# Performance work log

Measured on AMD Instinct MI355X. Metric: run time of the kernel, lower is better.

## Reference

```python
import jax, jax.numpy as jnp
import numpy as np

# DoG parameters derived from init kwargs: sigma_low=1.0, truncate=4.0
SIGMA_LOW = 1.0
SIGMA_HIGH = 1.6  # sigma_low * 1.6
KSIZE_LOW = 9     # 2*ceil(4.0*1.0)+1
KSIZE_HIGH = 15   # 2*ceil(4.0*1.6)+1


def gaussian_kernel1d(ksize: int, sigma: float) -> jnp.ndarray:
    # Matches kornia's 1D gaussian: centered, normalized to sum 1.
    t = jnp.arange(ksize, dtype=jnp.float32) - (ksize - 1) / 2.0
    g = jnp.exp(-(t * t) / (2.0 * sigma * sigma))
    return g / jnp.sum(g)


def _conv1d_along_axis(x: jnp.ndarray, g: jnp.ndarray, axis: int) -> jnp.ndarray:
    # x: (B, C, D, H, W); depthwise 1D cross-correlation along `axis` with
    # replicate ('edge') boundary handling, as in kornia filter3d(border_type='replicate').
    C = x.shape[1]
    k = g.shape[0]
    pads = [(0, 0)] * 5
    pads[axis] = (k // 2, k // 2)
    xp = jnp.pad(x, pads, mode='edge')
    kshape = [1, 1, 1]
    kshape[axis - 2] = k
    w = jnp.tile(g.reshape(1, 1, *kshape), (C, 1, 1, 1, 1))  # (C,1,kd,kh,kw)
    return jax.lax.conv_general_dilated(
        xp, w, window_strides=(1, 1, 1), padding='VALID',
        dimension_numbers=('NCDHW', 'OIDHW', 'NCDHW'),
        feature_group_count=C)


def gaussian_blur3d(x: jnp.ndarray, sigma: float, ksize: int) -> jnp.ndarray:
    # The 3D kernel is an outer product of normalized 1D gaussians, so the
    # dense 3D convolution is exactly equal to three separable 1D passes.
    g = gaussian_kernel1d(ksize, sigma)
    for ax in (2, 3, 4):
        x = _conv1d_along_axis(x, g, ax)
    return x


def setup_inputs() -> dict:
    key = jax.random.key(0)
    x = jax.random.normal(key, (2, 1, 160, 160, 160), dtype=jnp.float32)
    return {"x": x}


def reference(x) -> jnp.ndarray:
    low_pass = gaussian_blur3d(x, SIGMA_LOW, KSIZE_LOW)
    high_pass = gaussian_blur3d(x, SIGMA_HIGH, KSIZE_HIGH)
    return low_pass - high_pass
```

## Files before the change

kernel.cpp:

```cpp
#include <hip/hip_runtime.h>
#include <math.h>

#define DIMS 160
#define PLANE (DIMS*DIMS)
#define NB 2
#define RH 7
#define RL 4
#define KH 15
#define KL 9
#define TSX 16
#define TSY 32
#define NTX (DIMS/TSX)
#define NTY (DIMS/TSY)
#define CZ 16
#define NCH (DIMS/CZ)
#define NSTEPS (CZ + 2*RH)
#define YHR (TSY + 2*RH)
#define YLR (TSY + 2*RL)
#define RAWSZ 1860
#define SH 50
#define SL 42
#define NBLK (NTX*NTY*NCH*NB)

struct DoGW { float gl[KL]; float gh[KH]; };

__device__ __forceinline__ int raw_off(int r) {
  const int x = r & 15;
  return r * 40 + ((8 * ((x >> 2) & 3) + (x & 3) - 8 * (x & 3)) & 31);
}

__global__ __launch_bounds__(512, 4)
void dog_v6(const float* __restrict__ X, float* __restrict__ out, DoGW w) {
  __shared__ float sRaw[2][RAWSZ];
  __shared__ float sXh[2][TSX * SH];
  __shared__ float sXl[2][TSX * SL];

  const int bid = blockIdx.x;
  const int xt = bid % NTX;
  const int yt = (bid / NTX) % NTY;
  const int zc = (bid / (NTX * NTY)) % NCH;
  const int b  = bid / (NTX * NTY * NCH);
  const int x0 = xt * TSX, y0 = yt * TSY, z0 = zc * CZ;
  const float* Xb = X + (size_t)b * DIMS * PLANE;
  const int tid = threadIdx.x;
  const bool xfast = (x0 >= 8) && (x0 + 24 <= DIMS);

  const bool l_on = tid < YHR * 8;
  const int lrow = tid >> 3, lq = tid & 7;
  const int lyg = min(max(y0 + lrow - RH, 0), DIMS - 1);
  const int lxb = x0 - 8 + 4 * lq;
  const int lof = raw_off(lrow) + 4 * lq;

  const bool x_on = tid < YHR * 4;
  const int xr = tid >> 2, xq = tid & 3;
  const int xof = raw_off(xr) + 4 * xq;
  const bool xlow = (xr >= 3) && (xr <= 42);

  const int cy = tid >> 4, cx = tid & 15;

  auto loadP = [&](int s, float4& v) {
    if (!l_on) return;
    const int zsrc = min(max(z0 - RH + s, 0), DIMS - 1);
    const float* rowp = Xb + ((size_t)zsrc * DIMS + lyg) * DIMS;
    if (xfast) {
      v = *(const float4*)(rowp + lxb);
    } else {
      v.x = rowp[min(max(lxb + 0, 0), DIMS - 1)];
      v.y = rowp[min(max(lxb + 1, 0), DIMS - 1)];
      v.z = rowp[min(max(lxb + 2, 0), DIMS - 1)];
      v.w = rowp[min(max(lxb + 3, 0), DIMS - 1)];
    }
  };
  auto stageP = [&](const float4& v, int buf) {
    if (!l_on) return;
    float* p = &sRaw[buf][lof];
    p[0] = v.x; p[1] = v.y; p[2] = v.z; p[3] = v.w;
  };

  float accH[KH], accL[KL + 3];
  #pragma unroll
  for (int i = 0; i < KH; ++i) accH[i] = 0.f;
  #pragma unroll
  for (int i = 0; i < KL + 3; ++i) accL[i] = 0.f;

  {
    float4 v;
    loadP(0, v);
    stageP(v, 0);
  }
  __syncthreads();

  #pragma unroll 2
  for (int s = 0; s < NSTEPS; ++s) {
    const int cur = s & 1;
    float4 vnext;
    if (s + 1 < NSTEPS) loadP(s + 1, vnext);

    if (x_on) {
      const float* p = &sRaw[cur][xof];
      float v[20];
      #pragma unroll
      for (int j = 0; j < 20; ++j) v[j] = p[j];
      #pragma unroll
      for (int c = 0; c < 4; ++c) {
        float a = 0.f;
        #pragma unroll
        for (int k = 0; k < KH; ++k) a = fmaf(w.gh[k], v[c + 1 + k], a);
        sXh[cur][(4 * xq + c) * SH + xr] = a;
      }
      if (xlow) {
        #pragma unroll
        for (int c = 0; c < 4; ++c) {
          float a = 0.f;
          #pragma unroll
          for (int k = 0; k < KL; ++k) a = fmaf(w.gl[k], v[c + 4 + k], a);
          sXl[cur][(4 * xq + c) * SL + (xr - 3)] = a;
        }
      }
    }
    if (s + 1 < NSTEPS) stageP(vnext, 1 - cur);

    __syncthreads();

    float ph = 0.f, pl = 0.f;
    #pragma unroll
    for (int j = 0; j < KH; ++j) ph = fmaf(w.gh[j], sXh[cur][cx * SH + cy + j], ph);
    #pragma unroll
    for (int j = 0; j < KL; ++j) pl = fmaf(w.gl[j], sXl[cur][cx * SL + cy + j], pl);

    #pragma unroll
    for (int i = 0; i < KH; ++i) accH[i] = fmaf(w.gh[KH - 1 - i], ph, accH[i]);
    #pragma unroll
    for (int i = 3; i < KL + 3; ++i) accL[i] = fmaf(w.gl[KL + 2 - i], pl, accL[i]);

    if (s >= 2 * RH) {
      const int zo = z0 + s - 2 * RH;
      out[((size_t)(b * DIMS + zo) * DIMS + (y0 + cy)) * DIMS + (x0 + cx)] = accL[0] - accH[0];
    }
    #pragma unroll
    for (int i = 0; i < KH - 1; ++i) accH[i] = accH[i + 1];
    accH[KH - 1] = 0.f;
    #pragma unroll
    for (int i = 0; i < KL + 2; ++i) accL[i] = accL[i + 1];
    accL[KL + 2] = 0.f;
  }
}

extern "C" void kernel_launch(void* const* d_in, const int* in_sizes, int n_in,
                              void* d_out, int out_size, void* d_ws, size_t ws_size,
                              hipStream_t stream) {
  const float* X = (const float*)d_in[0];
  float* out = (float*)d_out;

  DoGW w;
  {
    double s = 0.0;
    for (int i = 0; i < KL; ++i) {
      double t = i - (KL - 1) / 2.0;
      double g = exp(-(t * t) / (2.0 * 1.0 * 1.0));
      w.gl[i] = (float)g; s += g;
    }
    for (int i = 0; i < KL; ++i) w.gl[i] = (float)((double)w.gl[i] / s);
    s = 0.0;
    for (int i = 0; i < KH; ++i) {
      double t = i - (KH - 1) / 2.0;
      double g = exp(-(t * t) / (2.0 * 1.6 * 1.6));
      w.gh[i] = (float)g; s += g;
    }
    for (int i = 0; i < KH; ++i) w.gh[i] = (float)((double)w.gh[i] / s);
  }

  dog_v6<<<NBLK, 512, 0, stream>>>(X, out, w);
}
```

Baseline: 143.0 us.

## Software-pipeline DoG stages with two-step global prefetch and skewed consume

The z-direction (and y) consume of step s-1 now runs in the same barrier interval as the x-convolution of step s. The global load for step s+2 is also issued while step s is processed, so each global read has two iterations to land. The aim is to hide global-memory latency and to fill the idle time around the per-step barrier with independent work. The cost is one more float4 held live across iterations, plus an epilogue consume after the loop, which may raise register pressure under the 512-thread launch bound.

```diff
diff --git a/kernel.cpp b/kernel.cpp
--- a/kernel.cpp
+++ b/kernel.cpp
@@ -30,7 +30,7 @@
 }
 
 __global__ __launch_bounds__(512, 4)
-void dog_v6(const float* __restrict__ X, float* __restrict__ out, DoGW w) {
+void dog_v7(const float* __restrict__ X, float* __restrict__ out, DoGW w) {
   __shared__ float sRaw[2][RAWSZ];
   __shared__ float sXh[2][TSX * SH];
   __shared__ float sXl[2][TSX * SL];
@@ -83,58 +83,19 @@
   #pragma unroll
   for (int i = 0; i < KL + 3; ++i) accL[i] = 0.f;
 
-  {
-    float4 v;
-    loadP(0, v);
-    stageP(v, 0);
-  }
-  __syncthreads();
-
-  #pragma unroll 2
-  for (int s = 0; s < NSTEPS; ++s) {
-    const int cur = s & 1;
-    float4 vnext;
-    if (s + 1 < NSTEPS) loadP(s + 1, vnext);
-
-    if (x_on) {
-      const float* p = &sRaw[cur][xof];
-      float v[20];
-      #pragma unroll
-      for (int j = 0; j < 20; ++j) v[j] = p[j];
-      #pragma unroll
-      for (int c = 0; c < 4; ++c) {
-        float a = 0.f;
-        #pragma unroll
-        for (int k = 0; k < KH; ++k) a = fmaf(w.gh[k], v[c + 1 + k], a);
-        sXh[cur][(4 * xq + c) * SH + xr] = a;
-      }
-      if (xlow) {
-        #pragma unroll
-        for (int c = 0; c < 4; ++c) {
-          float a = 0.f;
-          #pragma unroll
-          for (int k = 0; k < KL; ++k) a = fmaf(w.gl[k], v[c + 4 + k], a);
-          sXl[cur][(4 * xq + c) * SL + (xr - 3)] = a;
-        }
-      }
-    }
-    if (s + 1 < NSTEPS) stageP(vnext, 1 - cur);
-
-    __syncthreads();
-
+  auto consumeQ = [&](int q) {
+    const int qb = q & 1;
     float ph = 0.f, pl = 0.f;
     #pragma unroll
-    for (int j = 0; j < KH; ++j) ph = fmaf(w.gh[j], sXh[cur][cx * SH + cy + j], ph);
+    for (int j = 0; j < KH; ++j) ph = fmaf(w.gh[j], sXh[qb][cx * SH + cy + j], ph);
     #pragma unroll
-    for (int j = 0; j < KL; ++j) pl = fmaf(w.gl[j], sXl[cur][cx * SL + cy + j], pl);
-
+    for (int j = 0; j < KL; ++j) pl = fmaf(w.gl[j], sXl[qb][cx * SL + cy + j], pl);
     #pragma unroll
     for (int i = 0; i < KH; ++i) accH[i] = fmaf(w.gh[KH - 1 - i], ph, accH[i]);
     #pragma unroll
     for (int i = 3; i < KL + 3; ++i) accL[i] = fmaf(w.gl[KL + 2 - i], pl, accL[i]);
-
-    if (s >= 2 * RH) {
-      const int zo = z0 + s - 2 * RH;
+    if (q >= 2 * RH) {
+      const int zo = z0 + q - 2 * RH;
       out[((size_t)(b * DIMS + zo) * DIMS + (y0 + cy)) * DIMS + (x0 + cx)] = accL[0] - accH[0];
     }
     #pragma unroll
@@ -143,7 +104,51 @@
     #pragma unroll
     for (int i = 0; i < KL + 2; ++i) accL[i] = accL[i + 1];
     accL[KL + 2] = 0.f;
+  };
+
+  auto xconvP = [&](int cur) {
+    if (!x_on) return;
+    const float* p = &sRaw[cur][xof];
+    float v[20];
+    #pragma unroll
+    for (int j = 0; j < 20; ++j) v[j] = p[j];
+    #pragma unroll
+    for (int c = 0; c < 4; ++c) {
+      float a = 0.f;
+      #pragma unroll
+      for (int k = 0; k < KH; ++k) a = fmaf(w.gh[k], v[c + 1 + k], a);
+      sXh[cur][(4 * xq + c) * SH + xr] = a;
+    }
+    if (xlow) {
+      #pragma unroll
+      for (int c = 0; c < 4; ++c) {
+        float a = 0.f;
+        #pragma unroll
+        for (int k = 0; k < KL; ++k) a = fmaf(w.gl[k], v[c + 4 + k], a);
+        sXl[cur][(4 * xq + c) * SL + (xr - 3)] = a;
+      }
+    }
+  };
+
+  float4 vH;
+  {
+    float4 v0;
+    loadP(0, v0);
+    stageP(v0, 0);
+    loadP(1, vH);
   }
+  __syncthreads();
+
+  #pragma unroll 2
+  for (int s = 0; s < NSTEPS; ++s) {
+    const int cur = s & 1;
+    if (s + 1 < NSTEPS) stageP(vH, 1 - cur);
+    if (s + 2 < NSTEPS) loadP(s + 2, vH);
+    if (s >= 1) consumeQ(s - 1);
+    xconvP(cur);
+    __syncthreads();
+  }
+  consumeQ(NSTEPS - 1);
 }
 
 extern "C" void kernel_launch(void* const* d_in, const int* in_sizes, int n_in,
@@ -170,5 +175,5 @@
     for (int i = 0; i < KH; ++i) w.gh[i] = (float)((double)w.gh[i] / s);
   }
 
-  dog_v6<<<NBLK, 512, 0, stream>>>(X, out, w);
+  dog_v7<<<NBLK, 512, 0, stream>>>(X, out, w);
 }
```

Result: faster. 134.7 us (-5.8%).
